# Optimization experiments

Measured on AMD Instinct MI355X. Metric: run time of the kernel, lower is better.

## Reference

```python
import jax, jax.numpy as jnp
import numpy as np

jax.config.update("jax_enable_x64", True)  # needed for faithful int64 topology hash (31**i weights)

B, SEQ, HID, OUT = 64, 2048, 1024, 1024
MAX_DEPTH = 3
MAX_NODES = 2 ** MAX_DEPTH - 1          # 7
MAX_LEAVES = 2 ** (MAX_DEPTH - 1)       # 4 leaf slots (nodes 3..6)
MAX_SHAPE_IDS = 256


def _gelu(x):
    return jax.nn.gelu(x, approximate=False)  # torch nn.GELU default = exact erf


def setup_inputs() -> dict:
    key = jax.random.key(0)
    ks = jax.random.split(key, 8)
    states = jax.random.normal(ks[0], (B, SEQ, HID), dtype=jnp.float32)

    rng = np.random.default_rng(0)
    lengths = rng.integers(SEQ // 2, SEQ, size=(B,)).astype(np.int64)
    # sorted segment boundaries within [0, lengths), first boundary at 0
    fr = np.sort(rng.random((B, MAX_LEAVES - 1)), axis=1)
    boundaries = np.concatenate(
        [np.zeros((B, 1), np.int64), np.floor(fr * lengths[:, None]).astype(np.int64)], axis=1)
    mask = np.arange(SEQ)[None, :] < lengths[:, None]
    # complete binary tree, depth 3: node 0 root, nodes 1-2 internal, 3-6 leaves
    leaf_order = np.tile(np.arange(MAX_NODES // 2, MAX_NODES, dtype=np.int64), (B, 1))
    active = np.ones((B, MAX_NODES), bool)
    is_leaf = np.concatenate([np.zeros((B, 3), bool), np.ones((B, 4), bool)], axis=1)
    left_child = np.array([1, 3, 5, -1, -1, -1, -1], np.int64)
    right_child = np.array([2, 4, 6, -1, -1, -1, -1], np.int64)
    depth = np.array([0, 1, 1, 2, 2, 2, 2], np.int64)

    def lin(k, fan_in, shape):
        return jax.random.normal(k, shape, dtype=jnp.float32) / np.sqrt(fan_in).astype(np.float32)

    W1 = lin(ks[1], HID, (HID, OUT)); b1 = jnp.zeros((OUT,), jnp.float32)
    W2 = lin(ks[2], OUT, (OUT, OUT)); b2 = jnp.zeros((OUT,), jnp.float32)
    Wm1 = lin(ks[3], 2 * OUT, (2 * OUT, OUT)); bm1 = jnp.zeros((OUT,), jnp.float32)
    Wm2 = lin(ks[4], OUT, (OUT, OUT)); bm2 = jnp.zeros((OUT,), jnp.float32)
    depth_embed = jax.random.normal(ks[5], (MAX_DEPTH, OUT), dtype=jnp.float32) * 0.02
    shape_embed = jax.random.normal(ks[6], (MAX_SHAPE_IDS, OUT), dtype=jnp.float32) * 0.02

    return dict(
        states=states, mask=jnp.asarray(mask), lengths=jnp.asarray(lengths),
        boundaries=jnp.asarray(boundaries), leaf_order=jnp.asarray(leaf_order),
        active=jnp.asarray(active), is_leaf=jnp.asarray(is_leaf),
        left_child=jnp.asarray(left_child), right_child=jnp.asarray(right_child),
        depth=jnp.asarray(depth),
        W1=W1, b1=b1, W2=W2, b2=b2, Wm1=Wm1, bm1=bm1, Wm2=Wm2, bm2=bm2,
        depth_embed=depth_embed, shape_embed=shape_embed)


def _forward(states, W1, b1, W2, b2, Wm1, bm1, Wm2, bm2, depth_embed, shape_embed,
             mask, lengths, boundaries, leaf_order, active, is_leaf,
             left_child, right_child, depth):
    b, seq, _ = states.shape
    S = boundaries.shape[1]
    max_nodes = left_child.shape[0]

    # ---- 1. vectorized ragged masked segment-mean pooling ----
    pos = jnp.arange(seq)
    # segment id per token: number of boundaries <= t, minus 1
    seg_id = (pos[None, None, :] >= boundaries[:, :, None]).sum(1) - 1      # (b, seq)
    valid = mask & (pos[None, :] < lengths[:, None]) & (seg_id >= 0)
    onehot = ((seg_id[:, :, None] == jnp.arange(S)[None, None, :])
              & valid[:, :, None]).astype(states.dtype)                     # (b, seq, S)
    cnt = onehot.sum(1)                                                     # (b, S)
    pooled = jnp.einsum('bts,bth->bsh', onehot, states) / jnp.clip(cnt, 1.0)[..., None]

    # ---- 2. encode segments + depth embedding, scatter to leaf slots ----
    enc = _gelu(pooled @ W1 + b1) @ W2 + b2                                 # (b, S, D)
    nidx = leaf_order                                                       # (b, S)
    nclip = jnp.maximum(nidx, 0)
    enc = enc + depth_embed[depth[nclip]]
    leaf_ok = (nidx >= 0) & jnp.take_along_axis(is_leaf, nclip, axis=1) & (cnt > 0)
    contrib = enc * leaf_ok[..., None].astype(enc.dtype)
    node_repr = jnp.zeros((b, max_nodes, enc.shape[-1]), enc.dtype)
    node_repr = node_repr.at[jnp.arange(b)[:, None], nclip].add(contrib)

    # ---- 3. bottom-up binary tree merge (loop over fixed small node count) ----
    for i in range(max_nodes - 1, -1, -1):
        lc = left_child[i]
        rc = right_child[i]
        is_int = active[:, i] & ~is_leaf[:, i]                              # (b,)
        l = jnp.take(node_repr, jnp.maximum(lc, 0), axis=1)                 # (b, D)
        r = jnp.take(node_repr, jnp.maximum(rc, 0), axis=1)
        merged = (_gelu(jnp.concatenate([l, r], axis=-1) @ Wm1 + bm1) @ Wm2 + bm2
                  + depth_embed[depth[i]])
        upd = is_int.any() & (lc != -1)
        newv = jnp.where(upd, merged * is_int[:, None].astype(merged.dtype),
                         node_repr[:, i])
        node_repr = node_repr.at[:, i].set(newv)

    # ---- 4. topology hash -> shape embedding ----
    pattern = active.astype(jnp.int64) * 2 + is_leaf.astype(jnp.int64)      # (b, nodes)
    weights = 31 ** jnp.arange(max_nodes, dtype=jnp.int64)
    hashed = (pattern * weights[None, :]).sum(1)
    shape_ids = jnp.abs(hashed) % shape_embed.shape[0]
    return node_repr[:, 0] + shape_embed[shape_ids]


def reference(states, mask, lengths, boundaries, leaf_order, active, is_leaf,
              left_child, right_child, depth,
              W1, b1, W2, b2, Wm1, bm1, Wm2, bm2, depth_embed, shape_embed):
    return _forward(states, W1, b1, W2, b2, Wm1, bm1, Wm2, bm2,
                    depth_embed, shape_embed, mask, lengths, boundaries,
                    leaf_order, active, is_leaf, left_child, right_child, depth)
```

## Files before the change

kernel.cpp:

```cpp
#include <hip/hip_runtime.h>
#include <cstdint>
#include <cstddef>

#define SEQ   2048
#define HID   1024
#define NBAT  64
#define NSEG  4
#define NNODE 7
#define TCHUNK 128

__device__ __forceinline__ float gelu_f(float x) {
  return 0.5f * x * (1.0f + erff(x * 0.7071067811865476f));
}

__global__ __launch_bounds__(256) void pool_kernel(
    const float* __restrict__ states, const int* __restrict__ boundaries,
    const int* __restrict__ lengths, float* __restrict__ pooled_sum)
{
  const int tc = blockIdx.x, b = blockIdx.y;
  const int tid = threadIdx.x;
  const int len = lengths[b];
  int bnd[5];
  bnd[0] = boundaries[b * 4 + 0];
  bnd[1] = boundaries[b * 4 + 1];
  bnd[2] = boundaries[b * 4 + 2];
  bnd[3] = boundaries[b * 4 + 3];
  bnd[4] = len;
  const int clo = tc * TCHUNK, chi = clo + TCHUNK;
  const float4* S = (const float4*)(states + (size_t)b * SEQ * HID);

  #pragma unroll
  for (int s = 0; s < NSEG; ++s) {
    int lo = bnd[s]     > clo ? bnd[s]     : clo;
    int hi = bnd[s + 1] < chi ? bnd[s + 1] : chi;
    if (lo >= hi) continue;
    float4 acc = make_float4(0.f, 0.f, 0.f, 0.f);
    int t = lo;
    for (; t + 4 <= hi; t += 4) {
      float4 v0 = S[(size_t)(t + 0) * (HID / 4) + tid];
      float4 v1 = S[(size_t)(t + 1) * (HID / 4) + tid];
      float4 v2 = S[(size_t)(t + 2) * (HID / 4) + tid];
      float4 v3 = S[(size_t)(t + 3) * (HID / 4) + tid];
      acc.x += (v0.x + v1.x) + (v2.x + v3.x);
      acc.y += (v0.y + v1.y) + (v2.y + v3.y);
      acc.z += (v0.z + v1.z) + (v2.z + v3.z);
      acc.w += (v0.w + v1.w) + (v2.w + v3.w);
    }
    for (; t < hi; ++t) {
      float4 v = S[(size_t)t * (HID / 4) + tid];
      acc.x += v.x; acc.y += v.y; acc.z += v.z; acc.w += v.w;
    }
    float* dst = pooled_sum + (size_t)(b * NSEG + s) * HID + tid * 4;
    atomicAdd(dst + 0, acc.x);
    atomicAdd(dst + 1, acc.y);
    atomicAdd(dst + 2, acc.z);
    atomicAdd(dst + 3, acc.w);
  }
}

#define BM 32
#define BN 64
#define BK 32

template<int AMODE, int EPI>
__global__ __launch_bounds__(256) void gemm_kernel(
    const float* __restrict__ A, const float* __restrict__ W,
    const float* __restrict__ bias, float* __restrict__ C,
    int M, int K,
    const int* __restrict__ boundaries, const int* __restrict__ lengths,
    const int* __restrict__ leaf_order, const int* __restrict__ active,
    const int* __restrict__ is_leaf, const int* __restrict__ depth,
    const int* __restrict__ left_child, const int* __restrict__ right_child,
    const float* __restrict__ dembed, const float* __restrict__ sembed,
    const float* __restrict__ node_in, float* __restrict__ node_out,
    int nodeA, int nodeB)
{
  const int N = 1024;
  __shared__ float As[BK][BM + 2];
  __shared__ float Ws[BK][BN];

  const int tid = threadIdx.x;
  const int n0 = blockIdx.x * BN;
  const int m0 = blockIdx.y * BM;

  const int am = tid >> 3;
  const int ak = (tid & 7) * 4;
  const int wk = tid >> 3;
  const int wn = (tid & 7) * 8;
  const int rm = (tid >> 4) * 2;
  const int cn = (tid & 15) * 4;

  float ainv = 1.0f;
  int lcn = 0, rcn = 0, arow_b = 0;
  if (AMODE == 1) {
    int m = m0 + am; int b = m >> 2; int s = m & 3;
    int bs = boundaries[b * 4 + s];
    int bn = (s < 3) ? boundaries[b * 4 + s + 1] : lengths[b];
    ainv = 1.0f / fmaxf((float)(bn - bs), 1.0f);
  } else if (AMODE == 2) {
    int mrow = m0 + am; int mi = mrow >> 6; int b = mrow & 63;
    int node = mi ? nodeB : nodeA;
    lcn = left_child[node]; rcn = right_child[node];
    arow_b = b;
  }

  float acc[2][4] = {{0.f,0.f,0.f,0.f},{0.f,0.f,0.f,0.f}};

  float4 av, wv0, wv1;
  {
    if (AMODE == 2) {
      int col = ak;
      int child = (col < 1024) ? lcn : rcn;
      av = *(const float4*)(node_in + (size_t)(arow_b * NNODE + child) * 1024 + (col & 1023));
    } else {
      av = *(const float4*)(A + (size_t)(m0 + am) * K + ak);
    }
    wv0 = *(const float4*)(W + (size_t)wk * N + n0 + wn);
    wv1 = *(const float4*)(W + (size_t)wk * N + n0 + wn + 4);
  }

  for (int k0 = 0; k0 < K; k0 += BK) {
    __syncthreads();
    As[ak + 0][am] = av.x * ainv;
    As[ak + 1][am] = av.y * ainv;
    As[ak + 2][am] = av.z * ainv;
    As[ak + 3][am] = av.w * ainv;
    *(float4*)&Ws[wk][wn]     = wv0;
    *(float4*)&Ws[wk][wn + 4] = wv1;
    __syncthreads();

    const int kn = k0 + BK;
    if (kn < K) {
      if (AMODE == 2) {
        int col = kn + ak;
        int child = (col < 1024) ? lcn : rcn;
        av = *(const float4*)(node_in + (size_t)(arow_b * NNODE + child) * 1024 + (col & 1023));
      } else {
        av = *(const float4*)(A + (size_t)(m0 + am) * K + kn + ak);
      }
      wv0 = *(const float4*)(W + (size_t)(kn + wk) * N + n0 + wn);
      wv1 = *(const float4*)(W + (size_t)(kn + wk) * N + n0 + wn + 4);
    }

    #pragma unroll
    for (int kk = 0; kk < BK; ++kk) {
      float2 a2 = *(const float2*)&As[kk][rm];
      float4 w  = *(const float4*)&Ws[kk][cn];
      acc[0][0] += a2.x * w.x; acc[0][1] += a2.x * w.y;
      acc[0][2] += a2.x * w.z; acc[0][3] += a2.x * w.w;
      acc[1][0] += a2.y * w.x; acc[1][1] += a2.y * w.y;
      acc[1][2] += a2.y * w.z; acc[1][3] += a2.y * w.w;
    }
  }

  #pragma unroll
  for (int r = 0; r < 2; ++r) {
    const int m = m0 + rm + r;
    const int n = n0 + cn;
    float4 x;
    x.x = acc[r][0] + bias[n + 0];
    x.y = acc[r][1] + bias[n + 1];
    x.z = acc[r][2] + bias[n + 2];
    x.w = acc[r][3] + bias[n + 3];

    if (EPI == 0) {
      x.x = gelu_f(x.x); x.y = gelu_f(x.y); x.z = gelu_f(x.z); x.w = gelu_f(x.w);
      *(float4*)(C + (size_t)m * N + n) = x;
    } else if (EPI == 1) {
      int b = m >> 2; int s = m & 3;
      int node  = leaf_order[b * 4 + s];
      int nclip = node < 0 ? 0 : node;
      int bs = boundaries[b * 4 + s];
      int bn = (s < 3) ? boundaries[b * 4 + s + 1] : lengths[b];
      bool ok = (node >= 0) && (is_leaf[b * NNODE + nclip] != 0) && (bn - bs > 0);
      int d = depth[nclip];
      const float* de = dembed + (size_t)d * 1024 + n;
      float sc = ok ? 1.0f : 0.0f;
      x.x = (x.x + de[0]) * sc; x.y = (x.y + de[1]) * sc;
      x.z = (x.z + de[2]) * sc; x.w = (x.w + de[3]) * sc;
      *(float4*)(node_out + (size_t)(b * NNODE + nclip) * 1024 + n) = x;
    } else if (EPI == 2) {
      int mi = m >> 6; int b = m & 63;
      int node = mi ? nodeB : nodeA;
      bool ii = (active[b * NNODE + node] != 0) && (is_leaf[b * NNODE + node] == 0);
      int d = depth[node];
      const float* de = dembed + (size_t)d * 1024 + n;
      float sc = ii ? 1.0f : 0.0f;
      x.x = (x.x + de[0]) * sc; x.y = (x.y + de[1]) * sc;
      x.z = (x.z + de[2]) * sc; x.w = (x.w + de[3]) * sc;
      *(float4*)(node_out + (size_t)(b * NNODE + node) * 1024 + n) = x;
    } else {
      int b = m & 63;
      bool ii = (active[b * NNODE + 0] != 0) && (is_leaf[b * NNODE + 0] == 0);
      int d = depth[0];
      const float* de = dembed + (size_t)d * 1024 + n;
      float sc = ii ? 1.0f : 0.0f;
      long long h = 0, w = 1;
      #pragma unroll
      for (int i = 0; i < NNODE; ++i) {
        long long p = (long long)active[b * NNODE + i] * 2
                    + (long long)is_leaf[b * NNODE + i];
        h += p * w;
        w *= 31;
      }
      long long a = h < 0 ? -h : h;
      int sid = (int)(a % 256);
      const float* se = sembed + (size_t)sid * 1024 + n;
      x.x = (x.x + de[0]) * sc + se[0];
      x.y = (x.y + de[1]) * sc + se[1];
      x.z = (x.z + de[2]) * sc + se[2];
      x.w = (x.w + de[3]) * sc + se[3];
      *(float4*)(node_out + (size_t)b * 1024 + n) = x;
    }
  }
}

extern "C" void kernel_launch(void* const* d_in, const int* in_sizes, int n_in,
                              void* d_out, int out_size, void* d_ws, size_t ws_size,
                              hipStream_t stream)
{
  const float* states     = (const float*)d_in[0];
  const int* lengths      = (const int*)d_in[2];
  const int* boundaries   = (const int*)d_in[3];
  const int* leaf_order   = (const int*)d_in[4];
  const int* active       = (const int*)d_in[5];
  const int* is_leaf      = (const int*)d_in[6];
  const int* left_child   = (const int*)d_in[7];
  const int* right_child  = (const int*)d_in[8];
  const int* depth        = (const int*)d_in[9];
  const float* W1  = (const float*)d_in[10];
  const float* b1  = (const float*)d_in[11];
  const float* W2  = (const float*)d_in[12];
  const float* b2  = (const float*)d_in[13];
  const float* Wm1 = (const float*)d_in[14];
  const float* bm1 = (const float*)d_in[15];
  const float* Wm2 = (const float*)d_in[16];
  const float* bm2 = (const float*)d_in[17];
  const float* dembed = (const float*)d_in[18];
  const float* sembed = (const float*)d_in[19];
  float* out = (float*)d_out;

  float* pooled    = (float*)d_ws;
  float* H1        = pooled + 256 * 1024;
  float* Hm        = H1 + 256 * 1024;
  float* node_repr = Hm + 128 * 1024;

  hipMemsetAsync(pooled, 0, (size_t)256 * 1024 * sizeof(float), stream);

  pool_kernel<<<dim3(SEQ / TCHUNK, NBAT), 256, 0, stream>>>(
      states, boundaries, lengths, pooled);

  gemm_kernel<1, 0><<<dim3(16, 8), 256, 0, stream>>>(
      pooled, W1, b1, H1, 256, 1024,
      boundaries, lengths, leaf_order, active, is_leaf, depth,
      left_child, right_child, dembed, sembed, nullptr, nullptr, -1, -1);

  gemm_kernel<0, 1><<<dim3(16, 8), 256, 0, stream>>>(
      H1, W2, b2, nullptr, 256, 1024,
      boundaries, lengths, leaf_order, active, is_leaf, depth,
      left_child, right_child, dembed, sembed, nullptr, node_repr, -1, -1);

  gemm_kernel<2, 0><<<dim3(16, 4), 256, 0, stream>>>(
      nullptr, Wm1, bm1, Hm, 128, 2048,
      boundaries, lengths, leaf_order, active, is_leaf, depth,
      left_child, right_child, dembed, sembed, node_repr, nullptr, 1, 2);
  gemm_kernel<0, 2><<<dim3(16, 4), 256, 0, stream>>>(
      Hm, Wm2, bm2, nullptr, 128, 1024,
      boundaries, lengths, leaf_order, active, is_leaf, depth,
      left_child, right_child, dembed, sembed, nullptr, node_repr, 1, 2);

  gemm_kernel<2, 0><<<dim3(16, 2), 256, 0, stream>>>(
      nullptr, Wm1, bm1, Hm, 64, 2048,
      boundaries, lengths, leaf_order, active, is_leaf, depth,
      left_child, right_child, dembed, sembed, node_repr, nullptr, 0, 0);
  gemm_kernel<0, 3><<<dim3(16, 2), 256, 0, stream>>>(
      Hm, Wm2, bm2, nullptr, 64, 1024,
      boundaries, lengths, leaf_order, active, is_leaf, depth,
      left_child, right_child, dembed, sembed, nullptr, out, 0, 0);
}
```

Measured before the change: 963.3 us.

## Replace FP32 SIMT GEMMs with split-bf16 MFMA GEMMs and weight preprocessing

```diff
diff --git a/kernel.cpp b/kernel.cpp
--- a/kernel.cpp
+++ b/kernel.cpp
@@ -9,8 +9,80 @@
 #define NNODE 7
 #define TCHUNK 128
 
+typedef __attribute__((ext_vector_type(8))) short short8;
+typedef __attribute__((ext_vector_type(8))) unsigned short ushort8;
+typedef __attribute__((ext_vector_type(4))) float f32x4;
+
 __device__ __forceinline__ float gelu_f(float x) {
   return 0.5f * x * (1.0f + erff(x * 0.7071067811865476f));
+}
+
+__device__ __forceinline__ void split1(float f, unsigned short& h, unsigned short& l) {
+  unsigned u = __float_as_uint(f);
+  h = (unsigned short)(u >> 16);
+  float hf = __uint_as_float(u & 0xFFFF0000u);
+  l = (unsigned short)(__float_as_uint(f - hf) >> 16);
+}
+
+__device__ __forceinline__ void split_f32x8(const float4 x0, const float4 x1, float s,
+                                            short8& hi, short8& lo) {
+  float v[8] = {x0.x * s, x0.y * s, x0.z * s, x0.w * s,
+                x1.x * s, x1.y * s, x1.z * s, x1.w * s};
+  #pragma unroll
+  for (int j = 0; j < 8; ++j) {
+    unsigned short h, l;
+    split1(v[j], h, l);
+    hi[j] = (short)h;
+    lo[j] = (short)l;
+  }
+}
+
+__global__ __launch_bounds__(256) void wprep_kernel(
+    const float* __restrict__ W1, const float* __restrict__ W2,
+    const float* __restrict__ Wm1, const float* __restrict__ Wm2,
+    unsigned short* __restrict__ o1h, unsigned short* __restrict__ o1l,
+    unsigned short* __restrict__ o2h, unsigned short* __restrict__ o2l,
+    unsigned short* __restrict__ om1h, unsigned short* __restrict__ om1l,
+    unsigned short* __restrict__ om2h, unsigned short* __restrict__ om2l)
+{
+  const float* src; unsigned short *dh, *dl; int K;
+  switch (blockIdx.z) {
+    case 0: src = W1;  dh = o1h;  dl = o1l;  K = 1024; break;
+    case 1: src = W2;  dh = o2h;  dl = o2l;  K = 1024; break;
+    case 2: src = Wm1; dh = om1h; dl = om1l; K = 2048; break;
+    default: src = Wm2; dh = om2h; dl = om2l; K = 1024; break;
+  }
+  const int k0 = blockIdx.x * 64;
+  if (k0 >= K) return;
+  const int n0 = blockIdx.y * 64;
+
+  __shared__ float T[64][65];
+  const int t = threadIdx.x;
+  const int lr = t >> 4, lc = (t & 15) * 4;
+  #pragma unroll
+  for (int i = 0; i < 4; ++i) {
+    int kk = lr + i * 16;
+    float4 v = *(const float4*)(src + (size_t)(k0 + kk) * 1024 + n0 + lc);
+    T[kk][lc + 0] = v.x; T[kk][lc + 1] = v.y;
+    T[kk][lc + 2] = v.z; T[kk][lc + 3] = v.w;
+  }
+  __syncthreads();
+
+  const int n = t >> 2, kc = (t & 3) * 16;
+  ushort8 h0, h1, l0, l1;
+  #pragma unroll
+  for (int j = 0; j < 8; ++j) {
+    unsigned short h, l;
+    split1(T[kc + j][n], h, l);
+    h0[j] = h; l0[j] = l;
+    split1(T[kc + 8 + j][n], h, l);
+    h1[j] = h; l1[j] = l;
+  }
+  size_t o = (size_t)(n0 + n) * K + k0 + kc;
+  *(ushort8*)(dh + o)     = h0;
+  *(ushort8*)(dh + o + 8) = h1;
+  *(ushort8*)(dl + o)     = l0;
+  *(ushort8*)(dl + o + 8) = l1;
 }
 
 __global__ __launch_bounds__(256) void pool_kernel(
@@ -19,13 +91,12 @@
 {
   const int tc = blockIdx.x, b = blockIdx.y;
   const int tid = threadIdx.x;
-  const int len = lengths[b];
   int bnd[5];
   bnd[0] = boundaries[b * 4 + 0];
   bnd[1] = boundaries[b * 4 + 1];
   bnd[2] = boundaries[b * 4 + 2];
   bnd[3] = boundaries[b * 4 + 3];
-  bnd[4] = len;
+  bnd[4] = lengths[b];
   const int clo = tc * TCHUNK, chi = clo + TCHUNK;
   const float4* S = (const float4*)(states + (size_t)b * SEQ * HID);
 
@@ -58,159 +129,164 @@
   }
 }
 
-#define BM 32
-#define BN 64
-#define BK 32
-
-template<int AMODE, int EPI>
-__global__ __launch_bounds__(256) void gemm_kernel(
-    const float* __restrict__ A, const float* __restrict__ W,
-    const float* __restrict__ bias, float* __restrict__ C,
-    int M, int K,
+template<int AMODE, int EPI, int KDIM>
+__global__ __launch_bounds__(256) void mfma_gemm(
+    const float* __restrict__ Af,
+    const unsigned short* __restrict__ Ah, const unsigned short* __restrict__ Al,
+    const unsigned short* __restrict__ Bh, const unsigned short* __restrict__ Bl,
+    const float* __restrict__ bias,
+    unsigned short* __restrict__ Ch, unsigned short* __restrict__ Cl,
+    float* __restrict__ Cf,
     const int* __restrict__ boundaries, const int* __restrict__ lengths,
     const int* __restrict__ leaf_order, const int* __restrict__ active,
     const int* __restrict__ is_leaf, const int* __restrict__ depth,
     const int* __restrict__ left_child, const int* __restrict__ right_child,
     const float* __restrict__ dembed, const float* __restrict__ sembed,
-    const float* __restrict__ node_in, float* __restrict__ node_out,
+    const unsigned short* __restrict__ nodeH, const unsigned short* __restrict__ nodeL,
     int nodeA, int nodeB)
 {
-  const int N = 1024;
-  __shared__ float As[BK][BM + 2];
-  __shared__ float Ws[BK][BN];
-
-  const int tid = threadIdx.x;
-  const int n0 = blockIdx.x * BN;
-  const int m0 = blockIdx.y * BM;
-
-  const int am = tid >> 3;
-  const int ak = (tid & 7) * 4;
-  const int wk = tid >> 3;
-  const int wn = (tid & 7) * 8;
-  const int rm = (tid >> 4) * 2;
-  const int cn = (tid & 15) * 4;
-
-  float ainv = 1.0f;
-  int lcn = 0, rcn = 0, arow_b = 0;
-  if (AMODE == 1) {
-    int m = m0 + am; int b = m >> 2; int s = m & 3;
-    int bs = boundaries[b * 4 + s];
-    int bn = (s < 3) ? boundaries[b * 4 + s + 1] : lengths[b];
-    ainv = 1.0f / fmaxf((float)(bn - bs), 1.0f);
-  } else if (AMODE == 2) {
-    int mrow = m0 + am; int mi = mrow >> 6; int b = mrow & 63;
-    int node = mi ? nodeB : nodeA;
-    lcn = left_child[node]; rcn = right_child[node];
-    arow_b = b;
-  }
-
-  float acc[2][4] = {{0.f,0.f,0.f,0.f},{0.f,0.f,0.f,0.f}};
-
-  float4 av, wv0, wv1;
-  {
-    if (AMODE == 2) {
-      int col = ak;
-      int child = (col < 1024) ? lcn : rcn;
-      av = *(const float4*)(node_in + (size_t)(arow_b * NNODE + child) * 1024 + (col & 1023));
-    } else {
-      av = *(const float4*)(A + (size_t)(m0 + am) * K + ak);
-    }
-    wv0 = *(const float4*)(W + (size_t)wk * N + n0 + wn);
-    wv1 = *(const float4*)(W + (size_t)wk * N + n0 + wn + 4);
-  }
-
-  for (int k0 = 0; k0 < K; k0 += BK) {
-    __syncthreads();
-    As[ak + 0][am] = av.x * ainv;
-    As[ak + 1][am] = av.y * ainv;
-    As[ak + 2][am] = av.z * ainv;
-    As[ak + 3][am] = av.w * ainv;
-    *(float4*)&Ws[wk][wn]     = wv0;
-    *(float4*)&Ws[wk][wn + 4] = wv1;
-    __syncthreads();
-
-    const int kn = k0 + BK;
-    if (kn < K) {
-      if (AMODE == 2) {
-        int col = kn + ak;
-        int child = (col < 1024) ? lcn : rcn;
-        av = *(const float4*)(node_in + (size_t)(arow_b * NNODE + child) * 1024 + (col & 1023));
-      } else {
-        av = *(const float4*)(A + (size_t)(m0 + am) * K + kn + ak);
-      }
-      wv0 = *(const float4*)(W + (size_t)(kn + wk) * N + n0 + wn);
-      wv1 = *(const float4*)(W + (size_t)(kn + wk) * N + n0 + wn + 4);
-    }
-
-    #pragma unroll
-    for (int kk = 0; kk < BK; ++kk) {
-      float2 a2 = *(const float2*)&As[kk][rm];
-      float4 w  = *(const float4*)&Ws[kk][cn];
-      acc[0][0] += a2.x * w.x; acc[0][1] += a2.x * w.y;
-      acc[0][2] += a2.x * w.z; acc[0][3] += a2.x * w.w;
-      acc[1][0] += a2.y * w.x; acc[1][1] += a2.y * w.y;
-      acc[1][2] += a2.y * w.z; acc[1][3] += a2.y * w.w;
-    }
-  }
-
-  #pragma unroll
-  for (int r = 0; r < 2; ++r) {
-    const int m = m0 + rm + r;
-    const int n = n0 + cn;
-    float4 x;
-    x.x = acc[r][0] + bias[n + 0];
-    x.y = acc[r][1] + bias[n + 1];
-    x.z = acc[r][2] + bias[n + 2];
-    x.w = acc[r][3] + bias[n + 3];
-
-    if (EPI == 0) {
-      x.x = gelu_f(x.x); x.y = gelu_f(x.y); x.z = gelu_f(x.z); x.w = gelu_f(x.w);
-      *(float4*)(C + (size_t)m * N + n) = x;
-    } else if (EPI == 1) {
-      int b = m >> 2; int s = m & 3;
-      int node  = leaf_order[b * 4 + s];
-      int nclip = node < 0 ? 0 : node;
+  const int tid  = threadIdx.x;
+  const int wave = tid >> 6, lane = tid & 63;
+  const int wm = (wave >> 1) * 32, wn = (wave & 1) * 32;
+  const int l15 = lane & 15, q = lane >> 4;
+  const int m0 = blockIdx.y * 64, n0 = blockIdx.x * 64;
+  const int kq0 = q * 8;
+
+  f32x4 acc[2][2] = {};
+
+  int mrow[2];
+  mrow[0] = m0 + wm + l15;
+  mrow[1] = mrow[0] + 16;
+
+  const float* arow[2] = {nullptr, nullptr};
+  const unsigned short *ahrow[2], *alrow[2];
+  const unsigned short *aLh[2], *aLl[2], *aRh[2], *aRl[2];
+  float ainv[2] = {1.0f, 1.0f};
+
+  #pragma unroll
+  for (int mt = 0; mt < 2; ++mt) {
+    if (AMODE == 1) {
+      int b = mrow[mt] >> 2, s = mrow[mt] & 3;
       int bs = boundaries[b * 4 + s];
       int bn = (s < 3) ? boundaries[b * 4 + s + 1] : lengths[b];
-      bool ok = (node >= 0) && (is_leaf[b * NNODE + nclip] != 0) && (bn - bs > 0);
-      int d = depth[nclip];
-      const float* de = dembed + (size_t)d * 1024 + n;
-      float sc = ok ? 1.0f : 0.0f;
-      x.x = (x.x + de[0]) * sc; x.y = (x.y + de[1]) * sc;
-      x.z = (x.z + de[2]) * sc; x.w = (x.w + de[3]) * sc;
-      *(float4*)(node_out + (size_t)(b * NNODE + nclip) * 1024 + n) = x;
-    } else if (EPI == 2) {
-      int mi = m >> 6; int b = m & 63;
-      int node = mi ? nodeB : nodeA;
-      bool ii = (active[b * NNODE + node] != 0) && (is_leaf[b * NNODE + node] == 0);
-      int d = depth[node];
-      const float* de = dembed + (size_t)d * 1024 + n;
-      float sc = ii ? 1.0f : 0.0f;
-      x.x = (x.x + de[0]) * sc; x.y = (x.y + de[1]) * sc;
-      x.z = (x.z + de[2]) * sc; x.w = (x.w + de[3]) * sc;
-      *(float4*)(node_out + (size_t)(b * NNODE + node) * 1024 + n) = x;
+      ainv[mt] = 1.0f / fmaxf((float)(bn - bs), 1.0f);
+      arow[mt] = Af + (size_t)mrow[mt] * KDIM;
+    } else if (AMODE == 0) {
+      ahrow[mt] = Ah + (size_t)mrow[mt] * KDIM;
+      alrow[mt] = Al + (size_t)mrow[mt] * KDIM;
     } else {
-      int b = m & 63;
-      bool ii = (active[b * NNODE + 0] != 0) && (is_leaf[b * NNODE + 0] == 0);
-      int d = depth[0];
-      const float* de = dembed + (size_t)d * 1024 + n;
-      float sc = ii ? 1.0f : 0.0f;
-      long long h = 0, w = 1;
+      int node = (mrow[mt] >> 6) ? nodeB : nodeA;
+      int b = mrow[mt] & 63;
+      int lc = left_child[node], rc = right_child[node];
+      aLh[mt] = nodeH + (size_t)(b * NNODE + lc) * 1024;
+      aLl[mt] = nodeL + (size_t)(b * NNODE + lc) * 1024;
+      aRh[mt] = nodeH + (size_t)(b * NNODE + rc) * 1024;
+      aRl[mt] = nodeL + (size_t)(b * NNODE + rc) * 1024;
+    }
+  }
+
+  const unsigned short *brh[2], *brl[2];
+  #pragma unroll
+  for (int nt = 0; nt < 2; ++nt) {
+    int n = n0 + wn + nt * 16 + l15;
+    brh[nt] = Bh + (size_t)n * KDIM;
+    brl[nt] = Bl + (size_t)n * KDIM;
+  }
+
+  #pragma unroll 4
+  for (int k0 = 0; k0 < KDIM; k0 += 32) {
+    const int kq = k0 + kq0;
+    short8 ah[2], al[2], bh[2], bl[2];
+    #pragma unroll
+    for (int mt = 0; mt < 2; ++mt) {
+      if (AMODE == 1) {
+        const float* rp = arow[mt] + kq;
+        float4 x0 = *(const float4*)rp;
+        float4 x1 = *(const float4*)(rp + 4);
+        split_f32x8(x0, x1, ainv[mt], ah[mt], al[mt]);
+      } else if (AMODE == 0) {
+        ah[mt] = *(const short8*)(ahrow[mt] + kq);
+        al[mt] = *(const short8*)(alrow[mt] + kq);
+      } else {
+        const bool L = (k0 < 1024);
+        const int c = kq & 1023;
+        ah[mt] = *(const short8*)((L ? aLh[mt] : aRh[mt]) + c);
+        al[mt] = *(const short8*)((L ? aLl[mt] : aRl[mt]) + c);
+      }
+    }
+    #pragma unroll
+    for (int nt = 0; nt < 2; ++nt) {
+      bh[nt] = *(const short8*)(brh[nt] + kq);
+      bl[nt] = *(const short8*)(brl[nt] + kq);
+    }
+    #pragma unroll
+    for (int mt = 0; mt < 2; ++mt)
       #pragma unroll
-      for (int i = 0; i < NNODE; ++i) {
-        long long p = (long long)active[b * NNODE + i] * 2
-                    + (long long)is_leaf[b * NNODE + i];
-        h += p * w;
-        w *= 31;
+      for (int nt = 0; nt < 2; ++nt) {
+        acc[mt][nt] = __builtin_amdgcn_mfma_f32_16x16x32_bf16(ah[mt], bh[nt], acc[mt][nt], 0, 0, 0);
+        acc[mt][nt] = __builtin_amdgcn_mfma_f32_16x16x32_bf16(ah[mt], bl[nt], acc[mt][nt], 0, 0, 0);
+        acc[mt][nt] = __builtin_amdgcn_mfma_f32_16x16x32_bf16(al[mt], bh[nt], acc[mt][nt], 0, 0, 0);
       }
-      long long a = h < 0 ? -h : h;
-      int sid = (int)(a % 256);
-      const float* se = sembed + (size_t)sid * 1024 + n;
-      x.x = (x.x + de[0]) * sc + se[0];
-      x.y = (x.y + de[1]) * sc + se[1];
-      x.z = (x.z + de[2]) * sc + se[2];
-      x.w = (x.w + de[3]) * sc + se[3];
-      *(float4*)(node_out + (size_t)b * 1024 + n) = x;
+  }
+
+  #pragma unroll
+  for (int mt = 0; mt < 2; ++mt) {
+    #pragma unroll
+    for (int nt = 0; nt < 2; ++nt) {
+      const int n = n0 + wn + nt * 16 + l15;
+      #pragma unroll
+      for (int r = 0; r < 4; ++r) {
+        const int m = m0 + wm + mt * 16 + q * 4 + r;
+        float x = acc[mt][nt][r] + bias[n];
+
+        if (EPI == 0) {
+          x = gelu_f(x);
+          unsigned short h, l;
+          split1(x, h, l);
+          Ch[(size_t)m * 1024 + n] = h;
+          Cl[(size_t)m * 1024 + n] = l;
+        } else if (EPI == 1) {
+          int b = m >> 2, s = m & 3;
+          int node  = leaf_order[b * 4 + s];
+          int nclip = node < 0 ? 0 : node;
+          int bs = boundaries[b * 4 + s];
+          int bn = (s < 3) ? boundaries[b * 4 + s + 1] : lengths[b];
+          bool ok = (node >= 0) && (is_leaf[b * NNODE + nclip] != 0) && (bn - bs > 0);
+          float sc = ok ? 1.0f : 0.0f;
+          x = (x + dembed[(size_t)depth[nclip] * 1024 + n]) * sc;
+          unsigned short h, l;
+          split1(x, h, l);
+          size_t o = (size_t)(b * NNODE + nclip) * 1024 + n;
+          Ch[o] = h; Cl[o] = l;
+        } else if (EPI == 2) {
+          int mi = m >> 6, b = m & 63;
+          int node = mi ? nodeB : nodeA;
+          bool ii = (active[b * NNODE + node] != 0) && (is_leaf[b * NNODE + node] == 0);
+          float sc = ii ? 1.0f : 0.0f;
+          x = (x + dembed[(size_t)depth[node] * 1024 + n]) * sc;
+          unsigned short h, l;
+          split1(x, h, l);
+          size_t o = (size_t)(b * NNODE + node) * 1024 + n;
+          Ch[o] = h; Cl[o] = l;
+        } else {
+          int b = m & 63;
+          bool ii = (active[b * NNODE + 0] != 0) && (is_leaf[b * NNODE + 0] == 0);
+          float sc = ii ? 1.0f : 0.0f;
+          long long hsh = 0, w = 1;
+          #pragma unroll
+          for (int i = 0; i < NNODE; ++i) {
+            long long p = (long long)active[b * NNODE + i] * 2
+                        + (long long)is_leaf[b * NNODE + i];
+            hsh += p * w;
+            w *= 31;
+          }
+          long long a = hsh < 0 ? -hsh : hsh;
+          int sid = (int)(a % 256);
+          x = (x + dembed[(size_t)depth[0] * 1024 + n]) * sc
+            + sembed[(size_t)sid * 1024 + n];
+          Cf[(size_t)b * 1024 + n] = x;
+        }
+      }
     }
   }
 }
@@ -240,41 +316,58 @@
   const float* sembed = (const float*)d_in[19];
   float* out = (float*)d_out;
 
-  float* pooled    = (float*)d_ws;
-  float* H1        = pooled + 256 * 1024;
-  float* Hm        = H1 + 256 * 1024;
-  float* node_repr = Hm + 128 * 1024;
-
-  hipMemsetAsync(pooled, 0, (size_t)256 * 1024 * sizeof(float), stream);
+  char* p = (char*)d_ws;
+  float* pooled = (float*)p;                 p += (size_t)256 * 1024 * 4;
+  unsigned short* H1h = (unsigned short*)p;  p += (size_t)256 * 1024 * 2;
+  unsigned short* H1l = (unsigned short*)p;  p += (size_t)256 * 1024 * 2;
+  unsigned short* Hmh = (unsigned short*)p;  p += (size_t)128 * 1024 * 2;
+  unsigned short* Hml = (unsigned short*)p;  p += (size_t)128 * 1024 * 2;
+  unsigned short* ndH = (unsigned short*)p;  p += (size_t)NBAT * NNODE * 1024 * 2;
+  unsigned short* ndL = (unsigned short*)p;  p += (size_t)NBAT * NNODE * 1024 * 2;
+  unsigned short* W1h = (unsigned short*)p;  p += (size_t)1024 * 1024 * 2;
+  unsigned short* W1l = (unsigned short*)p;  p += (size_t)1024 * 1024 * 2;
+  unsigned short* W2h = (unsigned short*)p;  p += (size_t)1024 * 1024 * 2;
+  unsigned short* W2l = (unsigned short*)p;  p += (size_t)1024 * 1024 * 2;
+  unsigned short* Wm1h = (unsigned short*)p; p += (size_t)1024 * 2048 * 2;
+  unsigned short* Wm1l = (unsigned short*)p; p += (size_t)1024 * 2048 * 2;
+  unsigned short* Wm2h = (unsigned short*)p; p += (size_t)1024 * 1024 * 2;
+  unsigned short* Wm2l = (unsigned short*)p; p += (size_t)1024 * 1024 * 2;
+
+  hipMemsetAsync(pooled, 0, (size_t)256 * 1024 * 4, stream);
+
+  wprep_kernel<<<dim3(32, 16, 4), 256, 0, stream>>>(
+      W1, W2, Wm1, Wm2, W1h, W1l, W2h, W2l, Wm1h, Wm1l, Wm2h, Wm2l);
 
   pool_kernel<<<dim3(SEQ / TCHUNK, NBAT), 256, 0, stream>>>(
       states, boundaries, lengths, pooled);
 
-  gemm_kernel<1, 0><<<dim3(16, 8), 256, 0, stream>>>(
-      pooled, W1, b1, H1, 256, 1024,
+  mfma_gemm<1, 0, 1024><<<dim3(16, 4), 256, 0, stream>>>(
+      pooled, nullptr, nullptr, W1h, W1l, b1, H1h, H1l, nullptr,
       boundaries, lengths, leaf_order, active, is_leaf, depth,
       left_child, right_child, dembed, sembed, nullptr, nullptr, -1, -1);
 
-  gemm_kernel<0, 1><<<dim3(16, 8), 256, 0, stream>>>(
-      H1, W2, b2, nullptr, 256, 1024,
-      boundaries, lengths, leaf_order, active, is_leaf, depth,
-      left_child, right_child, dembed, sembed, nullptr, node_repr, -1, -1);
-
-  gemm_kernel<2, 0><<<dim3(16, 4), 256, 0, stream>>>(
-      nullptr, Wm1, bm1, Hm, 128, 2048,
-      boundaries, lengths, leaf_order, active, is_leaf, depth,
-      left_child, right_child, dembed, sembed, node_repr, nullptr, 1, 2);
-  gemm_kernel<0, 2><<<dim3(16, 4), 256, 0, stream>>>(
-      Hm, Wm2, bm2, nullptr, 128, 1024,
-      boundaries, lengths, leaf_order, active, is_leaf, depth,
-      left_child, right_child, dembed, sembed, nullptr, node_repr, 1, 2);
-
-  gemm_kernel<2, 0><<<dim3(16, 2), 256, 0, stream>>>(
-      nullptr, Wm1, bm1, Hm, 64, 2048,
-      boundaries, lengths, leaf_order, active, is_leaf, depth,
-      left_child, right_child, dembed, sembed, node_repr, nullptr, 0, 0);
-  gemm_kernel<0, 3><<<dim3(16, 2), 256, 0, stream>>>(
-      Hm, Wm2, bm2, nullptr, 64, 1024,
-      boundaries, lengths, leaf_order, active, is_leaf, depth,
-      left_child, right_child, dembed, sembed, nullptr, out, 0, 0);
-}
+  mfma_gemm<0, 1, 1024><<<dim3(16, 4), 256, 0, stream>>>(
+      nullptr, H1h, H1l, W2h, W2l, b2, ndH, ndL, nullptr,
+      boundaries, lengths, leaf_order, active, is_leaf, depth,
+      left_child, right_child, dembed, sembed, nullptr, nullptr, -1, -1);
+
+  mfma_gemm<2, 0, 2048><<<dim3(16, 2), 256, 0, stream>>>(
+      nullptr, nullptr, nullptr, Wm1h, Wm1l, bm1, Hmh, Hml, nullptr,
+      boundaries, lengths, leaf_order, active, is_leaf, depth,
+      left_child, right_child, dembed, sembed, ndH, ndL, 1, 2);
+
+  mfma_gemm<0, 2, 1024><<<dim3(16, 2), 256, 0, stream>>>(
+      nullptr, Hmh, Hml, Wm2h, Wm2l, bm2, ndH, ndL, nullptr,
+      boundaries, lengths, leaf_order, active, is_leaf, depth,
+      left_child, right_child, dembed, sembed, nullptr, nullptr, 1, 2);
+
+  mfma_gemm<2, 0, 2048><<<dim3(16, 1), 256, 0, stream>>>(
+      nullptr, nullptr, nullptr, Wm1h, Wm1l, bm1, Hmh, Hml, nullptr,
+      boundaries, lengths, leaf_order, active, is_leaf, depth,
+      left_child, right_child, dembed, sembed, ndH, ndL, 0, 0);
+
+  mfma_gemm<0, 3, 1024><<<dim3(16, 1), 256, 0, stream>>>(
+      nullptr, Hmh, Hml, Wm2h, Wm2l, bm2, nullptr, nullptr, out,
+      boundaries, lengths, leaf_order, active, is_leaf, depth,
+      left_child, right_child, dembed, sembed, nullptr, nullptr, 0, 0);
+}
```

Result: slower. 1.018 ms (+5.7%).
